# Performance work log

Hardware: AMD Instinct MI355X
Metric: run time of the kernel (lower is better)

## Reference

```python
import jax, jax.numpy as jnp
import numpy as np

B, S, T = 512, 1024, 64

def setup_inputs() -> dict:
    key = jax.random.key(0)
    k1, k2, k3 = jax.random.split(key, 3)
    emissions = jax.random.normal(k1, (B, S, T), dtype=jnp.float32)
    tags = jax.random.randint(k2, (B, S), 0, T, dtype=jnp.int32)
    mask = jnp.ones((B, S), dtype=jnp.float32)
    transitions = jax.random.normal(k3, (T, T), dtype=jnp.float32)
    return {"emissions": emissions, "tags": tags, "mask": mask, "transitions": transitions}

def _gold_score(emissions, tags, mask, transitions):
    # emit score of the gold tag at each position: (B, S)
    e = jnp.take_along_axis(emissions, tags[:, :, None], axis=2)[:, :, 0]
    # NOTE: original indexes transitions[curr, prev]
    trans = transitions[tags[:, 1:], tags[:, :-1]]  # (B, S-1)
    score = e[:, 0] * mask[:, 0]
    score = score + jnp.sum((trans + e[:, 1:]) * mask[:, 1:], axis=1)
    return score

def _partition(emissions, mask, transitions):
    # init: emissions at t=0, masked (matches original, which multiplies score by mask[:,0])
    score0 = emissions[:, 0] * mask[:, 0][:, None]  # (B, T)
    emis_rest = jnp.swapaxes(emissions[:, 1:], 0, 1)  # (S-1, B, T)
    mask_rest = jnp.swapaxes(mask[:, 1:], 0, 1)       # (S-1, B)

    def step(score, xs):
        emit, m = xs  # (B, T), (B,)
        # next[b, j] = logsumexp_i(score[b, i] + transitions[i, j])
        nxt = jax.nn.logsumexp(score[:, :, None] + transitions[None, :, :], axis=1)
        score = nxt + emit * m[:, None]
        return score, None

    score, _ = jax.lax.scan(step, score0, (emis_rest, mask_rest))
    return jax.nn.logsumexp(score, axis=1)  # (B,)

def reference(emissions, tags, mask, transitions):
    gold = _gold_score(emissions, tags, mask, transitions)
    fwd = _partition(emissions, mask, transitions)
    return jnp.mean(fwd - gold)
```

## Files before the change

kernel.cpp:

```cpp
#include <hip/hip_runtime.h>

#define BB 512
#define SS 1024
#define TT 64

__device__ __forceinline__ float wsum64(float v) {
#pragma unroll
  for (int off = 32; off > 0; off >>= 1) v += __shfl_xor(v, off, 64);
  return v;
}

#define E_LIST(M) \
  M(0) M(1) M(2) M(3) M(4) M(5) M(6) M(7) \
  M(8) M(9) M(10) M(11) M(12) M(13) M(14) M(15) \
  M(16) M(17) M(18) M(19) M(20) M(21) M(22) M(23) \
  M(24) M(25) M(26) M(27) M(28) M(29) M(30) M(31) \
  M(32) M(33) M(34) M(35) M(36) M(37) M(38) M(39) \
  M(40) M(41) M(42) M(43) M(44) M(45) M(46) M(47) \
  M(48) M(49) M(50) M(51) M(52) M(53) M(54) M(55) \
  M(56) M(57) M(58) M(59) M(60) M(61) M(62) M(63)

#define RL(i) __int_as_float(__builtin_amdgcn_readlane(pb_, (i)))

#define FMA4(i0, i1, i2, i3)          \
  a0 = fmaf(RL(i0), E##i0, a0);       \
  a1 = fmaf(RL(i1), E##i1, a1);       \
  a2 = fmaf(RL(i2), E##i2, a2);       \
  a3 = fmaf(RL(i3), E##i3, a3);

#define FMA_ALL                      \
  FMA4(0, 1, 2, 3)                   \
  FMA4(4, 5, 6, 7)                   \
  FMA4(8, 9, 10, 11)                 \
  FMA4(12, 13, 14, 15)               \
  FMA4(16, 17, 18, 19)               \
  FMA4(20, 21, 22, 23)               \
  FMA4(24, 25, 26, 27)               \
  FMA4(28, 29, 30, 31)               \
  FMA4(32, 33, 34, 35)               \
  FMA4(36, 37, 38, 39)               \
  FMA4(40, 41, 42, 43)               \
  FMA4(44, 45, 46, 47)               \
  FMA4(48, 49, 50, 51)               \
  FMA4(52, 53, 54, 55)               \
  FMA4(56, 57, 58, 59)               \
  FMA4(60, 61, 62, 63)

#define CRF_STEP(ev, mkv)                                                           \
  do {                                                                              \
    float f_ = __expf((ev) * (mkv));                                                \
    float pv_ = (DIR == 1) ? p * (f_ * inv) : p;                                    \
    int pb_ = __float_as_int(pv_);                                                  \
    float a0 = 0.f, a1 = 0.f, a2 = 0.f, a3 = 0.f;                                   \
    FMA_ALL                                                                         \
    float s_ = (a0 + a1) + (a2 + a3);                                               \
    p = (DIR == 0) ? s_ * (f_ * inv) : s_;                                          \
    float rn_ = __int_as_float(__builtin_amdgcn_readfirstlane(__float_as_int(s_))); \
    inv = __builtin_amdgcn_rcpf(rn_);                                               \
    float lg_ = __logf(rn_);                                                        \
    Lacc += lg_;                                                                    \
    lastlg = lg_;                                                                   \
  } while (0)

template <int DIR>
__device__ __forceinline__ void part_run(int b, int lane, const float* __restrict__ em,
                                         const float* __restrict__ mask,
                                         const float* __restrict__ trans,
                                         float* __restrict__ outv) {
  const float* tp = trans + (DIR == 0 ? lane : lane * TT);
#define EINIT(i) float E##i = __expf((DIR == 0) ? tp[(i)*TT] : tp[(i)]);
  E_LIST(EINIT)
#undef EINIT

  const float* emb = em + (size_t)b * SS * TT;
  const float* mkb = mask + (size_t)b * SS;

  constexpr int NST = (DIR == 0) ? (SS / 2 - 1) : (SS / 2);
  constexpr int S0 = (DIR == 0) ? 1 : (SS - 1);
  constexpr int SD = (DIR == 0) ? 1 : -1;
  constexpr int NG8 = NST / 8;
  constexpr int TAIL8 = NST & 7;

  float p = (DIR == 0) ? __expf(emb[lane] * mkb[0]) : 1.0f;
  float inv = 1.0f, Lacc = 0.0f, lastlg = 0.0f;

  float ebuf[8];
#pragma unroll
  for (int k = 0; k < 8; ++k) ebuf[k] = emb[(S0 + SD * k) * TT + lane];
  const float* ep = emb + (ptrdiff_t)(S0 + SD * 8) * TT + lane;

  float mv = 0.f;
  for (int t8 = 0; t8 < NG8; ++t8) {
    if ((t8 & 7) == 0) mv = mkb[S0 + SD * (t8 * 8 + lane)];
    int base = (t8 & 7) * 8;
#pragma unroll
    for (int k = 0; k < 8; ++k) {
      float e = ebuf[k];
      ebuf[k] = *ep;
      ep += SD * TT;
      float mk = __int_as_float(
          __builtin_amdgcn_readlane(__float_as_int(mv), base + k));
      CRF_STEP(e, mk);
    }
  }
  if constexpr (TAIL8 > 0) {
#pragma unroll
    for (int k = 0; k < TAIL8; ++k) {
      float e = ebuf[k];
      float mk = __int_as_float(
          __builtin_amdgcn_readlane(__float_as_int(mv), (NG8 & 7) * 8 + k));
      CRF_STEP(e, mk);
    }
  }

  outv[b * TT + lane] = __logf(p) + (Lacc - lastlg);
}

__global__ void __launch_bounds__(64, 1)
    fused_kernel(const float* __restrict__ em, const int* __restrict__ tags,
                 const float* __restrict__ mask, const float* __restrict__ trans,
                 float* __restrict__ alpha, float* __restrict__ beta,
                 float* __restrict__ gpart) {
  const int lane = threadIdx.x;
  const int bid = blockIdx.x;
  if (bid < 2 * BB) {
    const int b = bid >> 1;
    if ((bid & 1) == 0)
      part_run<0>(b, lane, em, mask, trans, alpha);
    else
      part_run<1>(b, lane, em, mask, trans, beta);
  } else {
    const int gid = bid - 2 * BB;
    const int b = gid >> 2, q = gid & 3;
    const int* tg = tags + b * SS;
    const float* mkb = mask + (size_t)b * SS;
    const float* emb = em + (size_t)b * SS * TT;
    float part = 0.f;
#pragma unroll
    for (int i = 0; i < 4; ++i) {
      int s = q * 256 + i * 64 + lane;
      int t1 = tg[s];
      float e = emb[s * TT + t1];
      float contrib = (s == 0) ? e : (trans[t1 * TT + tg[s - 1]] + e);
      part = fmaf(contrib, mkb[s], part);
    }
    part = wsum64(part);
    if (lane == 0) gpart[gid] = part;
  }
}

__global__ void combine_kernel(const float* __restrict__ alpha, const float* __restrict__ beta,
                               const float* __restrict__ gpart, float* __restrict__ out) {
  const int b = threadIdx.x;
  const float* av = alpha + b * TT;
  const float* bv = beta + b * TT;
  float m = -3.4e38f, s = 0.f;
#pragma unroll 8
  for (int j = 0; j < TT; ++j) {
    float v = av[j] + bv[j];
    float nm = fmaxf(m, v);
    s = s * __expf(m - nm) + __expf(v - nm);
    m = nm;
  }
  float Z = m + __logf(s);
  float g = gpart[4 * b] + gpart[4 * b + 1] + gpart[4 * b + 2] + gpart[4 * b + 3];
  float val = Z - g;
  val = wsum64(val);
  __shared__ float red[8];
  if ((threadIdx.x & 63) == 0) red[threadIdx.x >> 6] = val;
  __syncthreads();
  if (threadIdx.x == 0) {
    float t = 0.f;
#pragma unroll
    for (int w = 0; w < 8; ++w) t += red[w];
    out[0] = t * (1.0f / (float)BB);
  }
}

extern "C" void kernel_launch(void* const* d_in, const int* in_sizes, int n_in,
                              void* d_out, int out_size, void* d_ws, size_t ws_size,
                              hipStream_t stream) {
  const float* em = (const float*)d_in[0];
  const int* tags = (const int*)d_in[1];
  const float* mask = (const float*)d_in[2];
  const float* trans = (const float*)d_in[3];
  float* out = (float*)d_out;

  float* alpha = (float*)d_ws;
  float* beta = alpha + BB * TT;
  float* gpart = beta + BB * TT;

  fused_kernel<<<2 * BB + 4 * BB, TT, 0, stream>>>(em, tags, mask, trans, alpha, beta, gpart);
  combine_kernel<<<1, BB, 0, stream>>>(alpha, beta, gpart, out);
}
```

Measured before the change: 326.2 us.

## Use fp16 dot2 for forward-backward matvec and parallelize combine reduction

The serial per-step 64x64 matvec now uses packed fp16 transition weights and v_dot2 instructions. Pairs of probabilities are gathered via DPP swap and packed into half2, which halves the readlane/FMA count per step. Probabilities are clamped to fit fp16 range and a 16x rescale is applied. The combine kernel is also spread across 64 blocks with wave-level reductions and an atomic add into a pre-zeroed output. This trades precision, with fp16 rounding accumulated over 512 steps, for a shorter latency-bound inner loop.

```diff
diff --git a/kernel.cpp b/kernel.cpp
--- a/kernel.cpp
+++ b/kernel.cpp
@@ -4,58 +4,64 @@
 #define SS 1024
 #define TT 64
 
+typedef _Float16 half2v __attribute__((ext_vector_type(2)));
+
+#if __has_builtin(__builtin_amdgcn_fdot2)
+#define FDOT2(a, b, c) __builtin_amdgcn_fdot2((a), (b), (c), false)
+#else
+#define FDOT2(a, b, c) ((c) + (float)(a)[0] * (float)(b)[0] + (float)(a)[1] * (float)(b)[1])
+#endif
+
 __device__ __forceinline__ float wsum64(float v) {
 #pragma unroll
   for (int off = 32; off > 0; off >>= 1) v += __shfl_xor(v, off, 64);
   return v;
 }
-
-#define E_LIST(M) \
+__device__ __forceinline__ float wmax64(float v) {
+#pragma unroll
+  for (int off = 32; off > 0; off >>= 1) v = fmaxf(v, __shfl_xor(v, off, 64));
+  return v;
+}
+
+#define H_LIST(M) \
   M(0) M(1) M(2) M(3) M(4) M(5) M(6) M(7) \
   M(8) M(9) M(10) M(11) M(12) M(13) M(14) M(15) \
   M(16) M(17) M(18) M(19) M(20) M(21) M(22) M(23) \
-  M(24) M(25) M(26) M(27) M(28) M(29) M(30) M(31) \
-  M(32) M(33) M(34) M(35) M(36) M(37) M(38) M(39) \
-  M(40) M(41) M(42) M(43) M(44) M(45) M(46) M(47) \
-  M(48) M(49) M(50) M(51) M(52) M(53) M(54) M(55) \
-  M(56) M(57) M(58) M(59) M(60) M(61) M(62) M(63)
-
-#define RL(i) __int_as_float(__builtin_amdgcn_readlane(pb_, (i)))
-
-#define FMA4(i0, i1, i2, i3)          \
-  a0 = fmaf(RL(i0), E##i0, a0);       \
-  a1 = fmaf(RL(i1), E##i1, a1);       \
-  a2 = fmaf(RL(i2), E##i2, a2);       \
-  a3 = fmaf(RL(i3), E##i3, a3);
-
-#define FMA_ALL                      \
-  FMA4(0, 1, 2, 3)                   \
-  FMA4(4, 5, 6, 7)                   \
-  FMA4(8, 9, 10, 11)                 \
-  FMA4(12, 13, 14, 15)               \
-  FMA4(16, 17, 18, 19)               \
-  FMA4(20, 21, 22, 23)               \
-  FMA4(24, 25, 26, 27)               \
-  FMA4(28, 29, 30, 31)               \
-  FMA4(32, 33, 34, 35)               \
-  FMA4(36, 37, 38, 39)               \
-  FMA4(40, 41, 42, 43)               \
-  FMA4(44, 45, 46, 47)               \
-  FMA4(48, 49, 50, 51)               \
-  FMA4(52, 53, 54, 55)               \
-  FMA4(56, 57, 58, 59)               \
-  FMA4(60, 61, 62, 63)
+  M(24) M(25) M(26) M(27) M(28) M(29) M(30) M(31)
+
+#define DOTG(g, acc)                                                   \
+  {                                                                    \
+    int sg_ = __builtin_amdgcn_readlane(pk_, 2 * (g));                 \
+    acc = FDOT2(__builtin_bit_cast(half2v, sg_), H##g, acc);           \
+  }
+
+#define DOT_ALL                                   \
+  DOTG(0, a0) DOTG(1, a1) DOTG(2, a2) DOTG(3, a3) \
+  DOTG(4, a0) DOTG(5, a1) DOTG(6, a2) DOTG(7, a3) \
+  DOTG(8, a0) DOTG(9, a1) DOTG(10, a2) DOTG(11, a3) \
+  DOTG(12, a0) DOTG(13, a1) DOTG(14, a2) DOTG(15, a3) \
+  DOTG(16, a0) DOTG(17, a1) DOTG(18, a2) DOTG(19, a3) \
+  DOTG(20, a0) DOTG(21, a1) DOTG(22, a2) DOTG(23, a3) \
+  DOTG(24, a0) DOTG(25, a1) DOTG(26, a2) DOTG(27, a3) \
+  DOTG(28, a0) DOTG(29, a1) DOTG(30, a2) DOTG(31, a3)
 
 #define CRF_STEP(ev, mkv)                                                           \
   do {                                                                              \
     float f_ = __expf((ev) * (mkv));                                                \
     float pv_ = (DIR == 1) ? p * (f_ * inv) : p;                                    \
-    int pb_ = __float_as_int(pv_);                                                  \
+    pv_ = fminf(pv_, 3.0e4f);                                                       \
+    int pi_ = __float_as_int(pv_);                                                  \
+    int ni_ = __builtin_amdgcn_update_dpp(0, pi_, 0xB1, 0xF, 0xF, true);            \
+    half2v pk2_;                                                                    \
+    pk2_[0] = (_Float16)pv_;                                                        \
+    pk2_[1] = (_Float16)__int_as_float(ni_);                                        \
+    int pk_ = __builtin_bit_cast(int, pk2_);                                        \
     float a0 = 0.f, a1 = 0.f, a2 = 0.f, a3 = 0.f;                                   \
-    FMA_ALL                                                                         \
-    float s_ = (a0 + a1) + (a2 + a3);                                               \
+    DOT_ALL                                                                         \
+    float s_ = fmaxf((a0 + a1) + (a2 + a3), 1e-30f);                                \
     p = (DIR == 0) ? s_ * (f_ * inv) : s_;                                          \
-    float rn_ = __int_as_float(__builtin_amdgcn_readfirstlane(__float_as_int(s_))); \
+    float rn_ =                                                                     \
+        16.0f * __int_as_float(__builtin_amdgcn_readfirstlane(__float_as_int(s_))); \
     inv = __builtin_amdgcn_rcpf(rn_);                                               \
     float lg_ = __logf(rn_);                                                        \
     Lacc += lg_;                                                                    \
@@ -68,9 +74,16 @@
                                          const float* __restrict__ trans,
                                          float* __restrict__ outv) {
   const float* tp = trans + (DIR == 0 ? lane : lane * TT);
-#define EINIT(i) float E##i = __expf((DIR == 0) ? tp[(i)*TT] : tp[(i)]);
-  E_LIST(EINIT)
-#undef EINIT
+#define HINIT(g)                                                          \
+  half2v H##g;                                                            \
+  {                                                                       \
+    float h0_ = __expf((DIR == 0) ? tp[(2 * (g)) * TT] : tp[2 * (g)]);    \
+    float h1_ = __expf((DIR == 0) ? tp[(2 * (g) + 1) * TT] : tp[2 * (g) + 1]); \
+    H##g[0] = (_Float16)h0_;                                              \
+    H##g[1] = (_Float16)h1_;                                              \
+  }
+  H_LIST(HINIT)
+#undef HINIT
 
   const float* emb = em + (size_t)b * SS * TT;
   const float* mkb = mask + (size_t)b * SS;
@@ -149,31 +162,28 @@
   }
 }
 
-__global__ void combine_kernel(const float* __restrict__ alpha, const float* __restrict__ beta,
-                               const float* __restrict__ gpart, float* __restrict__ out) {
-  const int b = threadIdx.x;
-  const float* av = alpha + b * TT;
-  const float* bv = beta + b * TT;
-  float m = -3.4e38f, s = 0.f;
-#pragma unroll 8
-  for (int j = 0; j < TT; ++j) {
-    float v = av[j] + bv[j];
-    float nm = fmaxf(m, v);
-    s = s * __expf(m - nm) + __expf(v - nm);
-    m = nm;
-  }
-  float Z = m + __logf(s);
-  float g = gpart[4 * b] + gpart[4 * b + 1] + gpart[4 * b + 2] + gpart[4 * b + 3];
-  float val = Z - g;
-  val = wsum64(val);
+__global__ void __launch_bounds__(512)
+    combine_kernel(const float* __restrict__ alpha, const float* __restrict__ beta,
+                   const float* __restrict__ gpart, float* __restrict__ out) {
+  const int w = threadIdx.x >> 6;
+  const int lane = threadIdx.x & 63;
+  const int b = blockIdx.x * 8 + w;
+  float v = alpha[b * TT + lane] + beta[b * TT + lane];
+  float m = wmax64(v);
+  float e = __expf(v - m);
+  e = wsum64(e);
   __shared__ float red[8];
-  if ((threadIdx.x & 63) == 0) red[threadIdx.x >> 6] = val;
+  if (lane == 0) {
+    float Z = m + __logf(e);
+    float g = gpart[4 * b] + gpart[4 * b + 1] + gpart[4 * b + 2] + gpart[4 * b + 3];
+    red[w] = Z - g;
+  }
   __syncthreads();
   if (threadIdx.x == 0) {
     float t = 0.f;
 #pragma unroll
-    for (int w = 0; w < 8; ++w) t += red[w];
-    out[0] = t * (1.0f / (float)BB);
+    for (int i = 0; i < 8; ++i) t += red[i];
+    atomicAdd(out, t * (1.0f / (float)BB));
   }
 }
 
@@ -190,6 +200,7 @@
   float* beta = alpha + BB * TT;
   float* gpart = beta + BB * TT;
 
+  hipMemsetAsync(d_out, 0, sizeof(float), stream);
   fused_kernel<<<2 * BB + 4 * BB, TT, 0, stream>>>(em, tags, mask, trans, alpha, beta, gpart);
-  combine_kernel<<<1, BB, 0, stream>>>(alpha, beta, gpart, out);
-}
+  combine_kernel<<<BB / 8, 512, 0, stream>>>(alpha, beta, gpart, out);
+}
```

Result: slower. 337.7 us (+3.5%).
